# Kernel tuning notes

Hardware: AMD Instinct MI355X
Metric: run time of the kernel (lower is better)

Reference implementation:

```python
import jax, jax.numpy as jnp
import numpy as np

B, S, N = 8, 32, 64
F_NODE = 32
TRI = N * (N - 1) // 2        # 2016 upper-triangular edge features per step
DIN = F_NODE + TRI            # 2048 GATConv input dim (node feats + broadcast edge feats)
H, DOUT = 4, 256              # num_heads, hidden_channels
R = 1024                      # rnn_hidden_size
OUT = TRI                     # edge_in_channels * N*(N-1)/2


def setup_inputs() -> dict:
    key = jax.random.key(0)
    ks = jax.random.split(key, 16)
    def nrm(k, shape, fan):
        return jax.random.normal(k, shape, jnp.float32) / np.float32(np.sqrt(fan))
    # complete directed graph (no self loops; GATConv adds them)
    idx = np.arange(N)
    src = np.repeat(idx, N); dst = np.tile(idx, N)
    keep = src != dst
    edge_index = jnp.asarray(np.stack([src[keep], dst[keep]]), dtype=jnp.int32)  # [2, 4032]
    return {
        "x_node": jax.random.normal(ks[0], (B, S, N, F_NODE), jnp.float32),
        "x_edge": jax.random.normal(ks[1], (B, S, TRI), jnp.float32),
        "edge_index": edge_index,
        "W_gat": nrm(ks[2], (DIN, H * DOUT), DIN),
        "att_src": nrm(ks[3], (H, DOUT), DOUT),
        "att_dst": nrm(ks[4], (H, DOUT), DOUT),
        "b_gat": jnp.zeros((DOUT,), jnp.float32),
        "W_ih0": nrm(ks[5], (3 * R, N * DOUT), N * DOUT),
        "W_hh0": nrm(ks[6], (3 * R, R), R),
        "b_ih0": jnp.zeros((3 * R,), jnp.float32),
        "b_hh0": jnp.zeros((3 * R,), jnp.float32),
        "W_ih1": nrm(ks[7], (3 * R, R), R),
        "W_hh1": nrm(ks[8], (3 * R, R), R),
        "b_ih1": jnp.zeros((3 * R,), jnp.float32),
        "b_hh1": jnp.zeros((3 * R,), jnp.float32),
        "W_fc": nrm(ks[9], (R, OUT), R),
        "b_fc": jnp.zeros((OUT,), jnp.float32),
    }


def _gru_layer(x, Wih, Whh, bih, bhh):
    # x: [B, S, D] -> [B, S, R], PyTorch GRU equations
    def step(h, xt):
        gi = xt @ Wih.T + bih
        gh = h @ Whh.T + bhh
        i_r, i_z, i_n = jnp.split(gi, 3, axis=-1)
        h_r, h_z, h_n = jnp.split(gh, 3, axis=-1)
        r = jax.nn.sigmoid(i_r + h_r)
        z = jax.nn.sigmoid(i_z + h_z)
        n = jnp.tanh(i_n + r * h_n)
        h = (1.0 - z) * n + z * h
        return h, h
    h0 = jnp.zeros((x.shape[0], Whh.shape[1]), x.dtype)
    _, ys = jax.lax.scan(step, h0, jnp.swapaxes(x, 0, 1))
    return jnp.swapaxes(ys, 0, 1)


def reference(x_node, x_edge, edge_index, W_gat, att_src, att_dst, b_gat,
              W_ih0, W_hh0, b_ih0, b_hh0, W_ih1, W_hh1, b_ih1, b_hh1, W_fc, b_fc):
    # concat node feats with per-step edge features broadcast to every node
    x = jnp.concatenate(
        [x_node, jnp.broadcast_to(x_edge[:, :, None, :], (B, S, N, TRI))], axis=-1)
    xg = x.reshape(B * S, N, DIN)                         # batch all (b,t) graphs
    h = (xg @ W_gat).reshape(B * S, N, H, DOUT)           # per-head projections
    a_s = jnp.einsum('bnhe,he->bnh', h, att_src)
    a_d = jnp.einsum('bnhe,he->bnh', h, att_dst)
    # edge (src j -> dst i): leaky_relu(a_src[j] + a_dst[i]); dense over [dst, src]
    scores = jax.nn.leaky_relu(a_d[:, :, None, :] + a_s[:, None, :, :], 0.2)  # [BS, i, j, H]
    adj = jnp.zeros((N, N), bool).at[edge_index[1], edge_index[0]].set(True)
    adj = adj.at[jnp.arange(N), jnp.arange(N)].set(True)  # GATConv add_self_loops=True
    scores = jnp.where(adj[None, :, :, None], scores, -jnp.inf)
    alpha = jax.nn.softmax(scores, axis=2)                # softmax over source neighbors
    gat = jnp.einsum('bish,bshe->bihe', alpha, h).mean(axis=2) + b_gat  # concat=False -> head mean
    gat = jax.nn.relu(gat)                                # [BS, N, DOUT]
    seq = gat.reshape(B, S, N * DOUT)
    y = _gru_layer(seq, W_ih0, W_hh0, b_ih0, b_hh0)
    y = _gru_layer(y, W_ih1, W_hh1, b_ih1, b_hh1)
    return y[:, -1] @ W_fc + b_fc                         # [B, OUT]
```

## Files before the change

### kernel.cpp

```cpp
#include <hip/hip_runtime.h>
#include <hip/hip_bf16.h>

using bf16 = __hip_bfloat16;
typedef __bf16 bf16x8 __attribute__((ext_vector_type(8)));
typedef float f32x4 __attribute__((ext_vector_type(4)));


__device__ __forceinline__ void unp2(unsigned int u, float& a, float& b) {
  a = __uint_as_float(u << 16);
  b = __uint_as_float(u & 0xffff0000u);
}

__device__ __forceinline__ bf16x8 cvt8(float4 a, float4 b) {
  bf16x8 r;
  r[0] = (__bf16)a.x; r[1] = (__bf16)a.y; r[2] = (__bf16)a.z; r[3] = (__bf16)a.w;
  r[4] = (__bf16)b.x; r[5] = (__bf16)b.y; r[6] = (__bf16)b.z; r[7] = (__bf16)b.w;
  return r;
}

__global__ __launch_bounds__(256) void gru_step2_k(
    const float* __restrict__ X,
    const float* __restrict__ Whh,
    const float* __restrict__ bhh,
    float* __restrict__ y,
    int s, int first) {
  __shared__ float hs[8][1024];
  const int tid = threadIdx.x;
  if (first) {
#pragma unroll
    for (int q = 0; q < 8; ++q) {
      int idx = q * 256 + tid;
      *(float4*)&hs[idx >> 8][(idx & 255) * 4] = make_float4(0.f, 0.f, 0.f, 0.f);
    }
  } else {
#pragma unroll
    for (int q = 0; q < 8; ++q) {
      int idx = q * 256 + tid;
      int b = idx >> 8, kf = (idx & 255) * 4;
      *(float4*)&hs[b][kf] =
          *(const float4*)&y[(size_t)(b * 32 + s - 1) * 1024 + kf];
    }
  }
  __syncthreads();
  const int wv = tid >> 6, lane = tid & 63;
  const int j = blockIdx.x * 4 + wv;
  const float* Wr = Whh + (size_t)j * 1024;
  const float* Wz = Whh + (size_t)(1024 + j) * 1024;
  const float* Wn = Whh + (size_t)(2048 + j) * 1024;
  float accR[8] = {}, accZ[8] = {}, accN[8] = {};
#pragma unroll
  for (int kk = 0; kk < 4; ++kk) {
    const int k = kk * 256 + lane * 4;
    float4 wr = *(const float4*)&Wr[k];
    float4 wz = *(const float4*)&Wz[k];
    float4 wn = *(const float4*)&Wn[k];
#pragma unroll
    for (int b = 0; b < 8; ++b) {
      float4 h4 = *(const float4*)&hs[b][k];
      accR[b] += h4.x * wr.x + h4.y * wr.y + h4.z * wr.z + h4.w * wr.w;
      accZ[b] += h4.x * wz.x + h4.y * wz.y + h4.z * wz.z + h4.w * wz.w;
      accN[b] += h4.x * wn.x + h4.y * wn.y + h4.z * wn.z + h4.w * wn.w;
    }
  }
#pragma unroll
  for (int d = 1; d < 64; d <<= 1) {
#pragma unroll
    for (int b = 0; b < 8; ++b) {
      accR[b] += __shfl_xor(accR[b], d);
      accZ[b] += __shfl_xor(accZ[b], d);
      accN[b] += __shfl_xor(accN[b], d);
    }
  }
  if (lane < 8) {
    const int b = lane;
    float sr = 0.f, sz = 0.f, sn = 0.f;
#pragma unroll
    for (int bb = 0; bb < 8; ++bb)
      if (b == bb) { sr = accR[bb]; sz = accZ[bb]; sn = accN[bb]; }
    const float* gip = X + (size_t)(b * 32 + s) * 3072;
    float r = 1.0f / (1.0f + __expf(-(gip[j] + sr + bhh[j])));
    float z = 1.0f / (1.0f + __expf(-(gip[1024 + j] + sz + bhh[1024 + j])));
    float n = tanhf(gip[2048 + j] + r * (sn + bhh[2048 + j]));
    float hp = hs[b][j];
    y[(size_t)(b * 32 + s) * 1024 + j] = (1.0f - z) * n + z * hp;
  }
}

__global__ __launch_bounds__(256) void gemm_bt16_k(const __bf16* __restrict__ A,
                                                   const float* __restrict__ Bm,
                                                   float* __restrict__ Cp,
                                                   int N, int K, int ksper) {
  __shared__ __bf16 As[256][40];
  __shared__ __bf16 Bs[128][40];
  const int tid = threadIdx.x;
  const int bn = blockIdx.x * 128;
  const int lane = tid & 63, wv = tid >> 6;
  const int wr = wv >> 1, wc = wv & 1;
  const int lr = lane & 15, kh = lane >> 4;
  const int brow = tid >> 1, bhalf = tid & 1;
  f32x4 acc[8][4] = {};
  const int kstot = K >> 5;
  int ks0 = blockIdx.z * ksper;
  int ks1 = ks0 + ksper; if (ks1 > kstot) ks1 = kstot;
  uint4 ra0, ra1, ra2, ra3; float4 rb0, rb1, rb2, rb3;
  {
    const int k0 = ks0 << 5;
    const uint4* ap = (const uint4*)(A + (size_t)tid * K + k0);
    ra0 = ap[0]; ra1 = ap[1]; ra2 = ap[2]; ra3 = ap[3];
    const float* bp = Bm + (size_t)(bn + brow) * K + k0 + bhalf * 16;
    rb0 = ((const float4*)bp)[0]; rb1 = ((const float4*)bp)[1];
    rb2 = ((const float4*)bp)[2]; rb3 = ((const float4*)bp)[3];
  }
  for (int ks = ks0; ks < ks1; ++ks) {
    __syncthreads();
    *(uint4*)&As[tid][0]  = ra0;
    *(uint4*)&As[tid][8]  = ra1;
    *(uint4*)&As[tid][16] = ra2;
    *(uint4*)&As[tid][24] = ra3;
    *(bf16x8*)&Bs[brow][bhalf * 16] = cvt8(rb0, rb1);
    *(bf16x8*)&Bs[brow][bhalf * 16 + 8] = cvt8(rb2, rb3);
    __syncthreads();
    if (ks + 1 < ks1) {
      const int k0 = (ks + 1) << 5;
      const uint4* ap = (const uint4*)(A + (size_t)tid * K + k0);
      ra0 = ap[0]; ra1 = ap[1]; ra2 = ap[2]; ra3 = ap[3];
      const float* bp = Bm + (size_t)(bn + brow) * K + k0 + bhalf * 16;
      rb0 = ((const float4*)bp)[0]; rb1 = ((const float4*)bp)[1];
      rb2 = ((const float4*)bp)[2]; rb3 = ((const float4*)bp)[3];
    }
    bf16x8 bfv[4];
#pragma unroll
    for (int ni = 0; ni < 4; ++ni)
      bfv[ni] = *(const bf16x8*)&Bs[wc * 64 + ni * 16 + lr][kh * 8];
#pragma unroll
    for (int mi = 0; mi < 8; ++mi) {
      bf16x8 af = *(const bf16x8*)&As[wr * 128 + mi * 16 + lr][kh * 8];
#pragma unroll
      for (int ni = 0; ni < 4; ++ni)
        acc[mi][ni] = __builtin_amdgcn_mfma_f32_16x16x32_bf16(af, bfv[ni],
                                                              acc[mi][ni], 0, 0, 0);
    }
  }
  float* cp = Cp + (size_t)blockIdx.z * 256 * N;
#pragma unroll
  for (int mi = 0; mi < 8; ++mi) {
#pragma unroll
    for (int ni = 0; ni < 4; ++ni) {
      const int row = wr * 128 + mi * 16 + kh * 4;
      const int col = bn + wc * 64 + ni * 16 + lr;
#pragma unroll
      for (int j = 0; j < 4; ++j)
        cp[(size_t)(row + j) * N + col] = acc[mi][ni][j];
    }
  }
}

template <bool BT>
__global__ __launch_bounds__(256) void mfma_gemm_k(const float* __restrict__ A,
                                                   const float* __restrict__ Bm,
                                                   float* __restrict__ Cp,
                                                   int M, int N, int K,
                                                   int lda, int ldb, int ksper) {
  __shared__ __bf16 As[128][40];
  __shared__ __bf16 Bs[128][40];
  const int tid = threadIdx.x;
  const int bm = blockIdx.y * 128, bn = blockIdx.x * 128;
  const int lane = tid & 63, wv = tid >> 6;
  const int wr = wv >> 1, wc = wv & 1;
  const int lr = lane & 15, kh = lane >> 4;
  f32x4 acc[4][4] = {};
  const int kstot = K >> 5;
  int ks0 = blockIdx.z * ksper;
  int ks1 = ks0 + ksper; if (ks1 > kstot) ks1 = kstot;
  for (int ks = ks0; ks < ks1; ++ks) {
    const int k0 = ks << 5;
    __syncthreads();
    {
      const int row = tid >> 1, half = tid & 1;
      const float* ap = A + (size_t)(bm + row) * lda + k0 + half * 16;
      float4 f0 = ((const float4*)ap)[0], f1 = ((const float4*)ap)[1];
      float4 f2 = ((const float4*)ap)[2], f3 = ((const float4*)ap)[3];
      *(bf16x8*)&As[row][half * 16] = cvt8(f0, f1);
      *(bf16x8*)&As[row][half * 16 + 8] = cvt8(f2, f3);
    }
    if (BT) {
      const int row = tid >> 1, half = tid & 1;
      const float* bp = Bm + (size_t)(bn + row) * ldb + k0 + half * 16;
      float4 f0 = ((const float4*)bp)[0], f1 = ((const float4*)bp)[1];
      float4 f2 = ((const float4*)bp)[2], f3 = ((const float4*)bp)[3];
      *(bf16x8*)&Bs[row][half * 16] = cvt8(f0, f1);
      *(bf16x8*)&Bs[row][half * 16 + 8] = cvt8(f2, f3);
    } else {
      const int kk = tid >> 3, ng = tid & 7;
      const float* bp = Bm + (size_t)(k0 + kk) * ldb + bn + ng * 16;
      float4 f[4];
#pragma unroll
      for (int q = 0; q < 4; ++q) f[q] = ((const float4*)bp)[q];
#pragma unroll
      for (int q = 0; q < 4; ++q) {
        Bs[ng * 16 + q * 4 + 0][kk] = (__bf16)f[q].x;
        Bs[ng * 16 + q * 4 + 1][kk] = (__bf16)f[q].y;
        Bs[ng * 16 + q * 4 + 2][kk] = (__bf16)f[q].z;
        Bs[ng * 16 + q * 4 + 3][kk] = (__bf16)f[q].w;
      }
    }
    __syncthreads();
    bf16x8 af[4], bfv[4];
#pragma unroll
    for (int mi = 0; mi < 4; ++mi)
      af[mi] = *(const bf16x8*)&As[wr * 64 + mi * 16 + lr][kh * 8];
#pragma unroll
    for (int ni = 0; ni < 4; ++ni)
      bfv[ni] = *(const bf16x8*)&Bs[wc * 64 + ni * 16 + lr][kh * 8];
#pragma unroll
    for (int mi = 0; mi < 4; ++mi)
#pragma unroll
      for (int ni = 0; ni < 4; ++ni)
        acc[mi][ni] = __builtin_amdgcn_mfma_f32_16x16x32_bf16(af[mi], bfv[ni],
                                                              acc[mi][ni], 0, 0, 0);
  }
  float* cp = Cp + (size_t)blockIdx.z * M * N;
#pragma unroll
  for (int mi = 0; mi < 4; ++mi) {
#pragma unroll
    for (int ni = 0; ni < 4; ++ni) {
      const int row = bm + wr * 64 + mi * 16 + kh * 4;
      const int col = bn + wc * 64 + ni * 16 + lr;
#pragma unroll
      for (int j = 0; j < 4; ++j)
        cp[(size_t)(row + j) * N + col] = acc[mi][ni][j];
    }
  }
}

__global__ __launch_bounds__(256) void reduce_k(const float* __restrict__ Cp,
                                                const float* __restrict__ bias,
                                                float* __restrict__ C,
                                                int MN, int N, int nsk) {
  int i = (blockIdx.x * 256 + threadIdx.x) * 4;
  if (i >= MN) return;
  float4 s = make_float4(0.f, 0.f, 0.f, 0.f);
  if (bias) s = *(const float4*)&bias[i % N];
  for (int sk = 0; sk < nsk; ++sk) {
    float4 p = *(const float4*)&Cp[(size_t)sk * MN + i];
    s.x += p.x; s.y += p.y; s.z += p.z; s.w += p.w;
  }
  *(float4*)&C[i] = s;
}

__global__ __launch_bounds__(256) void node_h_k(const float* __restrict__ xn,
                                                const float* __restrict__ Wg,
                                                const float* __restrict__ he,
                                                bf16* __restrict__ hbuf) {
  __shared__ float xns[64][32];
  __shared__ float wgs[32][256];
  const int cq = blockIdx.x, g = blockIdx.y;
  const int tid = threadIdx.x;
  for (int idx = tid; idx < 2048; idx += 256) xns[idx >> 5][idx & 31] = xn[g * 2048 + idx];
  for (int r = 0; r < 32; ++r) wgs[r][tid] = Wg[r * 1024 + cq * 256 + tid];
  __syncthreads();
  const float hev = he[g * 1024 + cq * 256 + tid];
  for (int n0 = 0; n0 < 64; n0 += 8) {
    float acc[8];
#pragma unroll
    for (int nn = 0; nn < 8; ++nn) acc[nn] = hev;
    for (int f = 0; f < 32; ++f) {
      float w = wgs[f][tid];
#pragma unroll
      for (int nn = 0; nn < 8; ++nn) acc[nn] += xns[n0 + nn][f] * w;
    }
#pragma unroll
    for (int nn = 0; nn < 8; ++nn)
      hbuf[(size_t)(g * 64 + n0 + nn) * 1024 + cq * 256 + tid] = __float2bfloat16(acc[nn]);
  }
}

__global__ __launch_bounds__(256) void as_ad_k(const bf16* __restrict__ hbuf,
                                               const float* __restrict__ att_s,
                                               const float* __restrict__ att_d,
                                               float* __restrict__ as_o,
                                               float* __restrict__ ad_o) {
  const int tid = threadIdx.x;
  const int lane = tid & 63, wv = tid >> 6;
  const int row = blockIdx.x * 4 + wv;
  const int hd = lane >> 4;
  const int e0 = (lane & 15) * 16;
  float as_r[16], ad_r[16];
#pragma unroll
  for (int q = 0; q < 4; ++q) {
    float4 v = *(const float4*)(att_s + hd * 256 + e0 + q * 4);
    as_r[q * 4 + 0] = v.x; as_r[q * 4 + 1] = v.y; as_r[q * 4 + 2] = v.z; as_r[q * 4 + 3] = v.w;
    float4 w = *(const float4*)(att_d + hd * 256 + e0 + q * 4);
    ad_r[q * 4 + 0] = w.x; ad_r[q * 4 + 1] = w.y; ad_r[q * 4 + 2] = w.z; ad_r[q * 4 + 3] = w.w;
  }
  const uint4* hp = (const uint4*)(hbuf + (size_t)row * 1024 + lane * 16);
  uint4 p0 = hp[0], p1 = hp[1];
  float hv[16];
  unp2(p0.x, hv[0], hv[1]);  unp2(p0.y, hv[2], hv[3]);
  unp2(p0.z, hv[4], hv[5]);  unp2(p0.w, hv[6], hv[7]);
  unp2(p1.x, hv[8], hv[9]);  unp2(p1.y, hv[10], hv[11]);
  unp2(p1.z, hv[12], hv[13]); unp2(p1.w, hv[14], hv[15]);
  float ps = 0.f, pd = 0.f;
#pragma unroll
  for (int i = 0; i < 16; ++i) { ps += as_r[i] * hv[i]; pd += ad_r[i] * hv[i]; }
#pragma unroll
  for (int m = 1; m < 16; m <<= 1) { ps += __shfl_xor(ps, m); pd += __shfl_xor(pd, m); }
  if ((lane & 15) == 0) { as_o[row * 4 + hd] = ps; ad_o[row * 4 + hd] = pd; }
}

__global__ __launch_bounds__(256) void attn_agg_k(const bf16* __restrict__ hbuf,
                                                  const float* __restrict__ as_i,
                                                  const float* __restrict__ ad_i,
                                                  const float* __restrict__ bgat,
                                                  __bf16* __restrict__ seq) {
  __shared__ float ass[256], ads[256], bgs[256];
  __shared__ float alpha[4][64][64];
  __shared__ float hq[64][260];
  const int g = blockIdx.x, tid = threadIdx.x;
  ass[tid] = as_i[g * 256 + tid];
  ads[tid] = ad_i[g * 256 + tid];
  bgs[tid] = bgat[tid];
  __syncthreads();
  {
    const int hd = tid >> 6, i = tid & 63;
    const float ad = ads[i * 4 + hd];
    float m = -1e30f;
    for (int j = 0; j < 64; ++j) {
      float s = ad + ass[j * 4 + hd];
      s = s > 0.0f ? s : 0.2f * s;
      m = fmaxf(m, s);
    }
    float sum = 0.0f;
    for (int j = 0; j < 64; ++j) {
      float s = ad + ass[j * 4 + hd];
      s = s > 0.0f ? s : 0.2f * s;
      sum += __expf(s - m);
    }
    const float inv = 1.0f / sum;
    for (int j = 0; j < 64; ++j) {
      float s = ad + ass[j * 4 + hd];
      s = s > 0.0f ? s : 0.2f * s;
      alpha[hd][j][i] = __expf(s - m) * inv;
    }
  }
  const int i = tid & 63, eq = tid >> 6;
  float acc[64] = {};
  for (int hd = 0; hd < 4; ++hd) {
    __syncthreads();
    for (int idx = tid; idx < 2048; idx += 256) {
      int j = idx >> 5, ch = idx & 31;
      uint4 p = *(const uint4*)(hbuf + (size_t)(g * 64 + j) * 1024 + hd * 256 + ch * 8);
      float f0, f1, f2, f3, f4, f5, f6, f7;
      unp2(p.x, f0, f1); unp2(p.y, f2, f3); unp2(p.z, f4, f5); unp2(p.w, f6, f7);
      *(float4*)&hq[j][ch * 8] = make_float4(f0, f1, f2, f3);
      *(float4*)&hq[j][ch * 8 + 4] = make_float4(f4, f5, f6, f7);
    }
    __syncthreads();
    for (int j = 0; j < 64; ++j) {
      const float a = alpha[hd][j][i];
      const float* hr = &hq[j][eq * 64];
#pragma unroll
      for (int q = 0; q < 16; ++q) {
        float4 hv = *(const float4*)(hr + q * 4);
        acc[q * 4 + 0] += a * hv.x; acc[q * 4 + 1] += a * hv.y;
        acc[q * 4 + 2] += a * hv.z; acc[q * 4 + 3] += a * hv.w;
      }
    }
  }
  __bf16* op = seq + (size_t)g * 16384 + i * 256 + eq * 64;
#pragma unroll
  for (int q = 0; q < 8; ++q) {
    float4 lo, hi;
    lo.x = fmaxf(bgs[eq * 64 + q * 8 + 0] + 0.25f * acc[q * 8 + 0], 0.0f);
    lo.y = fmaxf(bgs[eq * 64 + q * 8 + 1] + 0.25f * acc[q * 8 + 1], 0.0f);
    lo.z = fmaxf(bgs[eq * 64 + q * 8 + 2] + 0.25f * acc[q * 8 + 2], 0.0f);
    lo.w = fmaxf(bgs[eq * 64 + q * 8 + 3] + 0.25f * acc[q * 8 + 3], 0.0f);
    hi.x = fmaxf(bgs[eq * 64 + q * 8 + 4] + 0.25f * acc[q * 8 + 4], 0.0f);
    hi.y = fmaxf(bgs[eq * 64 + q * 8 + 5] + 0.25f * acc[q * 8 + 5], 0.0f);
    hi.z = fmaxf(bgs[eq * 64 + q * 8 + 6] + 0.25f * acc[q * 8 + 6], 0.0f);
    hi.w = fmaxf(bgs[eq * 64 + q * 8 + 7] + 0.25f * acc[q * 8 + 7], 0.0f);
    *(bf16x8*)(op + q * 8) = cvt8(lo, hi);
  }
}

__global__ __launch_bounds__(256) void fc_k(const float* __restrict__ y1,
                                            const float* __restrict__ Wfc,
                                            const float* __restrict__ bfc,
                                            float* __restrict__ out) {
  __shared__ float As[8][1024];
  const int tid = threadIdx.x;
  for (int idx = tid; idx < 8192; idx += 256) {
    int b = idx >> 10, k = idx & 1023;
    As[b][k] = y1[(size_t)(b * 32 + 31) * 1024 + k];
  }
  __syncthreads();
  const int ol = tid >> 2, kq = tid & 3;
  const int o = blockIdx.x * 64 + ol;
  float acc[8] = {};
  if (o < 2016) {
    for (int i2 = 0; i2 < 256; ++i2) {
      int k = i2 * 4 + kq;
      float w = Wfc[(size_t)k * 2016 + o];
#pragma unroll
      for (int b = 0; b < 8; ++b) acc[b] += As[b][k] * w;
    }
  }
#pragma unroll
  for (int b = 0; b < 8; ++b) {
    acc[b] += __shfl_xor(acc[b], 1);
    acc[b] += __shfl_xor(acc[b], 2);
  }
  if (kq == 0 && o < 2016) {
#pragma unroll
    for (int b = 0; b < 8; ++b) out[b * 2016 + o] = acc[b] + bfc[o];
  }
}

extern "C" void kernel_launch(void* const* d_in, const int* in_sizes, int n_in,
                              void* d_out, int out_size, void* d_ws, size_t ws_size,
                              hipStream_t stream) {
  (void)in_sizes; (void)n_in; (void)out_size; (void)ws_size;
  const float* x_node = (const float*)d_in[0];
  const float* x_edge = (const float*)d_in[1];
  const float* W_gat = (const float*)d_in[3];
  const float* att_s = (const float*)d_in[4];
  const float* att_d = (const float*)d_in[5];
  const float* b_gat = (const float*)d_in[6];
  const float* W_ih0 = (const float*)d_in[7];
  const float* W_hh0 = (const float*)d_in[8];
  const float* b_ih0 = (const float*)d_in[9];
  const float* b_hh0 = (const float*)d_in[10];
  const float* W_ih1 = (const float*)d_in[11];
  const float* W_hh1 = (const float*)d_in[12];
  const float* b_ih1 = (const float*)d_in[13];
  const float* b_hh1 = (const float*)d_in[14];
  const float* W_fc  = (const float*)d_in[15];
  const float* b_fc  = (const float*)d_in[16];

  char* ws = (char*)d_ws;
  size_t off = 0;
  float*  he  = (float*)(ws + off);  off += 256u * 1024 * 4;
  float*  a_s = (float*)(ws + off);  off += 256u * 64 * 4 * 4;
  float*  a_d = (float*)(ws + off);  off += 256u * 64 * 4 * 4;
  bf16*   hb  = (bf16*)(ws + off);   off += 256u * 64 * 1024 * 2;
  __bf16* seq = (__bf16*)(ws + off); off += 256u * 16384 * 2;
  float*  X0  = (float*)(ws + off);  off += 256u * 3072 * 4;
  float*  y0  = (float*)(ws + off);  off += 256u * 1024 * 4;
  float*  X1  = (float*)(ws + off);  off += 256u * 3072 * 4;
  float*  y1  = (float*)(ws + off);  off += 256u * 1024 * 4;
  off = (off + 255) & ~(size_t)255;
  float*  Cp  = (float*)(ws + off);  off += (size_t)16 * 256 * 3072 * 4;

  mfma_gemm_k<false><<<dim3(8, 2, 8), 256, 0, stream>>>(
      x_edge, W_gat + 32 * 1024, Cp, 256, 1024, 2016, 2016, 1024, 8);
  reduce_k<<<256, 256, 0, stream>>>(Cp, nullptr, he, 256 * 1024, 1024, 8);
  node_h_k<<<dim3(4, 256), 256, 0, stream>>>(x_node, W_gat, he, hb);
  as_ad_k<<<4096, 256, 0, stream>>>(hb, att_s, att_d, a_s, a_d);
  attn_agg_k<<<256, 256, 0, stream>>>(hb, a_s, a_d, b_gat, seq);
  gemm_bt16_k<<<dim3(24, 1, 16), 256, 0, stream>>>(seq, W_ih0, Cp,
                                                   3072, 16384, 32);
  reduce_k<<<768, 256, 0, stream>>>(Cp, b_ih0, X0, 256 * 3072, 3072, 16);
  for (int s = 0; s < 32; ++s)
    gru_step2_k<<<256, 256, 0, stream>>>(X0, W_hh0, b_hh0, y0, s, s == 0 ? 1 : 0);
  mfma_gemm_k<true><<<dim3(24, 2, 4), 256, 0, stream>>>(
      y0, W_ih1, Cp, 256, 3072, 1024, 1024, 1024, 8);
  reduce_k<<<768, 256, 0, stream>>>(Cp, b_ih1, X1, 256 * 3072, 3072, 4);
  for (int s = 0; s < 32; ++s)
    gru_step2_k<<<256, 256, 0, stream>>>(X1, W_hh1, b_hh1, y1, s, s == 0 ? 1 : 0);
  fc_k<<<32, 256, 0, stream>>>(y1, W_fc, b_fc, (float*)d_out);
}
```

Baseline: 665.6 us.

## Replace per-step GRU launches with persistent kernel using grid barrier

The 32 per-timestep GRU kernel launches per layer become one persistent kernel that loops over timesteps. Blocks synchronise through a flag-based grid barrier in global memory, with block 0 acting as the releaser, which removes per-launch overhead and relaunch gaps. The bf16 GEMM k-loop is also restructured into a two-stage ping-pong register prefetch. The barrier relies on all 256 blocks being co-resident, which holds on this GPU but would deadlock otherwise. Its relaxed atomics carry no explicit fences, so the ordering of the y writes is not guaranteed by the memory model.

Result: slower. 852.2 us (+28.0%).

```diff
diff --git a/kernel.cpp b/kernel.cpp
--- a/kernel.cpp
+++ b/kernel.cpp
@@ -18,71 +18,106 @@
   return r;
 }
 
-__global__ __launch_bounds__(256) void gru_step2_k(
+__device__ __forceinline__ float ald(const float* p) {
+  return __hip_atomic_load(p, __ATOMIC_RELAXED, __HIP_MEMORY_SCOPE_AGENT);
+}
+__device__ __forceinline__ void ast(float* p, float v) {
+  __hip_atomic_store(p, v, __ATOMIC_RELAXED, __HIP_MEMORY_SCOPE_AGENT);
+}
+__device__ __forceinline__ unsigned uald(const unsigned* p) {
+  return __hip_atomic_load(p, __ATOMIC_RELAXED, __HIP_MEMORY_SCOPE_AGENT);
+}
+__device__ __forceinline__ void uast(unsigned* p, unsigned v) {
+  __hip_atomic_store(p, v, __ATOMIC_RELAXED, __HIP_MEMORY_SCOPE_AGENT);
+}
+
+__global__ __launch_bounds__(256) void gru_persist2_k(
     const float* __restrict__ X,
     const float* __restrict__ Whh,
     const float* __restrict__ bhh,
     float* __restrict__ y,
-    int s, int first) {
+    unsigned* __restrict__ flags,
+    unsigned* __restrict__ rel) {
   __shared__ float hs[8][1024];
   const int tid = threadIdx.x;
-  if (first) {
-#pragma unroll
-    for (int q = 0; q < 8; ++q) {
-      int idx = q * 256 + tid;
-      *(float4*)&hs[idx >> 8][(idx & 255) * 4] = make_float4(0.f, 0.f, 0.f, 0.f);
-    }
-  } else {
-#pragma unroll
-    for (int q = 0; q < 8; ++q) {
-      int idx = q * 256 + tid;
-      int b = idx >> 8, kf = (idx & 255) * 4;
-      *(float4*)&hs[b][kf] =
-          *(const float4*)&y[(size_t)(b * 32 + s - 1) * 1024 + kf];
-    }
-  }
-  __syncthreads();
+  const int bid = blockIdx.x;
   const int wv = tid >> 6, lane = tid & 63;
-  const int j = blockIdx.x * 4 + wv;
+  const int j = bid * 4 + wv;
   const float* Wr = Whh + (size_t)j * 1024;
   const float* Wz = Whh + (size_t)(1024 + j) * 1024;
   const float* Wn = Whh + (size_t)(2048 + j) * 1024;
-  float accR[8] = {}, accZ[8] = {}, accN[8] = {};
-#pragma unroll
-  for (int kk = 0; kk < 4; ++kk) {
-    const int k = kk * 256 + lane * 4;
-    float4 wr = *(const float4*)&Wr[k];
-    float4 wz = *(const float4*)&Wz[k];
-    float4 wn = *(const float4*)&Wn[k];
-#pragma unroll
-    for (int b = 0; b < 8; ++b) {
-      float4 h4 = *(const float4*)&hs[b][k];
-      accR[b] += h4.x * wr.x + h4.y * wr.y + h4.z * wr.z + h4.w * wr.w;
-      accZ[b] += h4.x * wz.x + h4.y * wz.y + h4.z * wz.z + h4.w * wz.w;
-      accN[b] += h4.x * wn.x + h4.y * wn.y + h4.z * wn.z + h4.w * wn.w;
-    }
-  }
-#pragma unroll
-  for (int d = 1; d < 64; d <<= 1) {
-#pragma unroll
-    for (int b = 0; b < 8; ++b) {
-      accR[b] += __shfl_xor(accR[b], d);
-      accZ[b] += __shfl_xor(accZ[b], d);
-      accN[b] += __shfl_xor(accN[b], d);
-    }
-  }
-  if (lane < 8) {
-    const int b = lane;
-    float sr = 0.f, sz = 0.f, sn = 0.f;
-#pragma unroll
-    for (int bb = 0; bb < 8; ++bb)
-      if (b == bb) { sr = accR[bb]; sz = accZ[bb]; sn = accN[bb]; }
-    const float* gip = X + (size_t)(b * 32 + s) * 3072;
-    float r = 1.0f / (1.0f + __expf(-(gip[j] + sr + bhh[j])));
-    float z = 1.0f / (1.0f + __expf(-(gip[1024 + j] + sz + bhh[1024 + j])));
-    float n = tanhf(gip[2048 + j] + r * (sn + bhh[2048 + j]));
-    float hp = hs[b][j];
-    y[(size_t)(b * 32 + s) * 1024 + j] = (1.0f - z) * n + z * hp;
+  const float bhr = bhh[j], bhz = bhh[1024 + j], bhn = bhh[2048 + j];
+  for (int s = 0; s < 32; ++s) {
+    if (s == 0) {
+#pragma unroll
+      for (int q = 0; q < 8; ++q) {
+        int idx = q * 256 + tid;
+        *(float4*)&hs[idx >> 8][(idx & 255) * 4] = make_float4(0.f, 0.f, 0.f, 0.f);
+      }
+    } else {
+#pragma unroll
+      for (int q = 0; q < 8; ++q) {
+        int idx = q * 256 + tid;
+        int b = idx >> 8, kf = (idx & 255) * 4;
+        const float* hp_ = y + (size_t)(b * 32 + s - 1) * 1024 + kf;
+        float4 v;
+        v.x = ald(hp_ + 0); v.y = ald(hp_ + 1);
+        v.z = ald(hp_ + 2); v.w = ald(hp_ + 3);
+        *(float4*)&hs[b][kf] = v;
+      }
+    }
+    __syncthreads();
+    float accR[8] = {}, accZ[8] = {}, accN[8] = {};
+#pragma unroll
+    for (int kk = 0; kk < 4; ++kk) {
+      const int k = kk * 256 + lane * 4;
+      float4 wr = *(const float4*)&Wr[k];
+      float4 wz = *(const float4*)&Wz[k];
+      float4 wn = *(const float4*)&Wn[k];
+#pragma unroll
+      for (int b = 0; b < 8; ++b) {
+        float4 h4 = *(const float4*)&hs[b][k];
+        accR[b] += h4.x * wr.x + h4.y * wr.y + h4.z * wr.z + h4.w * wr.w;
+        accZ[b] += h4.x * wz.x + h4.y * wz.y + h4.z * wz.z + h4.w * wz.w;
+        accN[b] += h4.x * wn.x + h4.y * wn.y + h4.z * wn.z + h4.w * wn.w;
+      }
+    }
+#pragma unroll
+    for (int d = 1; d < 64; d <<= 1) {
+#pragma unroll
+      for (int b = 0; b < 8; ++b) {
+        accR[b] += __shfl_xor(accR[b], d);
+        accZ[b] += __shfl_xor(accZ[b], d);
+        accN[b] += __shfl_xor(accN[b], d);
+      }
+    }
+    if (lane < 8) {
+      const int b = lane;
+      float sr = 0.f, sz = 0.f, sn = 0.f;
+#pragma unroll
+      for (int bb = 0; bb < 8; ++bb)
+        if (b == bb) { sr = accR[bb]; sz = accZ[bb]; sn = accN[bb]; }
+      const float* gip = X + (size_t)(b * 32 + s) * 3072;
+      float r = 1.0f / (1.0f + __expf(-(gip[j] + sr + bhr)));
+      float z = 1.0f / (1.0f + __expf(-(gip[1024 + j] + sz + bhz)));
+      float n = tanhf(gip[2048 + j] + r * (sn + bhn));
+      float hp = hs[b][j];
+      ast(&y[(size_t)(b * 32 + s) * 1024 + j], (1.0f - z) * n + z * hp);
+    }
+    if (s < 31) {
+      const unsigned ep = (unsigned)(s + 1);
+      __syncthreads();
+      if (tid == 0) uast(&flags[bid * 16], ep);
+      if (bid == 0) {
+        while (uald(&flags[tid * 16]) != ep) __builtin_amdgcn_s_sleep(1);
+        __syncthreads();
+        if (tid == 0) uast(&rel[s * 16], 1u);
+      }
+      if (tid == 0) {
+        while (uald(&rel[s * 16]) == 0u) __builtin_amdgcn_s_sleep(1);
+      }
+      __syncthreads();
+    }
   }
 }
 
@@ -99,35 +134,41 @@
   const int lr = lane & 15, kh = lane >> 4;
   const int brow = tid >> 1, bhalf = tid & 1;
   f32x4 acc[8][4] = {};
-  const int kstot = K >> 5;
-  int ks0 = blockIdx.z * ksper;
-  int ks1 = ks0 + ksper; if (ks1 > kstot) ks1 = kstot;
-  uint4 ra0, ra1, ra2, ra3; float4 rb0, rb1, rb2, rb3;
-  {
-    const int k0 = ks0 << 5;
+  const int ks0 = blockIdx.z * ksper;
+  const int ks1 = ks0 + ksper;
+
+  uint4 xa0, xa1, xa2, xa3; float4 xb0, xb1, xb2, xb3;
+  uint4 ya0, ya1, ya2, ya3; float4 yb0, yb1, yb2, yb3;
+
+  auto loadX = [&](int ks) {
+    const int k0 = ks << 5;
     const uint4* ap = (const uint4*)(A + (size_t)tid * K + k0);
-    ra0 = ap[0]; ra1 = ap[1]; ra2 = ap[2]; ra3 = ap[3];
+    xa0 = ap[0]; xa1 = ap[1]; xa2 = ap[2]; xa3 = ap[3];
     const float* bp = Bm + (size_t)(bn + brow) * K + k0 + bhalf * 16;
-    rb0 = ((const float4*)bp)[0]; rb1 = ((const float4*)bp)[1];
-    rb2 = ((const float4*)bp)[2]; rb3 = ((const float4*)bp)[3];
-  }
-  for (int ks = ks0; ks < ks1; ++ks) {
-    __syncthreads();
-    *(uint4*)&As[tid][0]  = ra0;
-    *(uint4*)&As[tid][8]  = ra1;
-    *(uint4*)&As[tid][16] = ra2;
-    *(uint4*)&As[tid][24] = ra3;
-    *(bf16x8*)&Bs[brow][bhalf * 16] = cvt8(rb0, rb1);
-    *(bf16x8*)&Bs[brow][bhalf * 16 + 8] = cvt8(rb2, rb3);
-    __syncthreads();
-    if (ks + 1 < ks1) {
-      const int k0 = (ks + 1) << 5;
-      const uint4* ap = (const uint4*)(A + (size_t)tid * K + k0);
-      ra0 = ap[0]; ra1 = ap[1]; ra2 = ap[2]; ra3 = ap[3];
-      const float* bp = Bm + (size_t)(bn + brow) * K + k0 + bhalf * 16;
-      rb0 = ((const float4*)bp)[0]; rb1 = ((const float4*)bp)[1];
-      rb2 = ((const float4*)bp)[2]; rb3 = ((const float4*)bp)[3];
-    }
+    xb0 = ((const float4*)bp)[0]; xb1 = ((const float4*)bp)[1];
+    xb2 = ((const float4*)bp)[2]; xb3 = ((const float4*)bp)[3];
+  };
+  auto loadY = [&](int ks) {
+    const int k0 = ks << 5;
+    const uint4* ap = (const uint4*)(A + (size_t)tid * K + k0);
+    ya0 = ap[0]; ya1 = ap[1]; ya2 = ap[2]; ya3 = ap[3];
+    const float* bp = Bm + (size_t)(bn + brow) * K + k0 + bhalf * 16;
+    yb0 = ((const float4*)bp)[0]; yb1 = ((const float4*)bp)[1];
+    yb2 = ((const float4*)bp)[2]; yb3 = ((const float4*)bp)[3];
+  };
+  auto storeX = [&]() {
+    *(uint4*)&As[tid][0]  = xa0; *(uint4*)&As[tid][8]  = xa1;
+    *(uint4*)&As[tid][16] = xa2; *(uint4*)&As[tid][24] = xa3;
+    *(bf16x8*)&Bs[brow][bhalf * 16] = cvt8(xb0, xb1);
+    *(bf16x8*)&Bs[brow][bhalf * 16 + 8] = cvt8(xb2, xb3);
+  };
+  auto storeY = [&]() {
+    *(uint4*)&As[tid][0]  = ya0; *(uint4*)&As[tid][8]  = ya1;
+    *(uint4*)&As[tid][16] = ya2; *(uint4*)&As[tid][24] = ya3;
+    *(bf16x8*)&Bs[brow][bhalf * 16] = cvt8(yb0, yb1);
+    *(bf16x8*)&Bs[brow][bhalf * 16 + 8] = cvt8(yb2, yb3);
+  };
+  auto mfmaLDS = [&]() {
     bf16x8 bfv[4];
 #pragma unroll
     for (int ni = 0; ni < 4; ++ni)
@@ -140,6 +181,21 @@
         acc[mi][ni] = __builtin_amdgcn_mfma_f32_16x16x32_bf16(af, bfv[ni],
                                                               acc[mi][ni], 0, 0, 0);
     }
+  };
+
+  loadX(ks0);
+  loadY(ks0 + 1);
+  for (int ks = ks0; ks < ks1; ks += 2) {
+    __syncthreads();
+    storeX();
+    __syncthreads();
+    { int nk = ks + 2; if (nk >= ks1) nk = ks1 - 1; loadX(nk); }
+    mfmaLDS();
+    __syncthreads();
+    storeY();
+    __syncthreads();
+    { int nk = ks + 3; if (nk >= ks1) nk = ks1 - 1; loadY(nk); }
+    mfmaLDS();
   }
   float* cp = Cp + (size_t)blockIdx.z * 256 * N;
 #pragma unroll
@@ -149,8 +205,8 @@
       const int row = wr * 128 + mi * 16 + kh * 4;
       const int col = bn + wc * 64 + ni * 16 + lr;
 #pragma unroll
-      for (int j = 0; j < 4; ++j)
-        cp[(size_t)(row + j) * N + col] = acc[mi][ni][j];
+      for (int jj = 0; jj < 4; ++jj)
+        cp[(size_t)(row + jj) * N + col] = acc[mi][ni][jj];
     }
   }
 }
@@ -449,6 +505,8 @@
   float*  X1  = (float*)(ws + off);  off += 256u * 3072 * 4;
   float*  y1  = (float*)(ws + off);  off += 256u * 1024 * 4;
   off = (off + 255) & ~(size_t)255;
+  unsigned* flags = (unsigned*)(ws + off); off += 256u * 64;
+  unsigned* rel   = (unsigned*)(ws + off); off += 32u * 64;
   float*  Cp  = (float*)(ws + off);  off += (size_t)16 * 256 * 3072 * 4;
 
   mfma_gemm_k<false><<<dim3(8, 2, 8), 256, 0, stream>>>(
@@ -460,12 +518,12 @@
   gemm_bt16_k<<<dim3(24, 1, 16), 256, 0, stream>>>(seq, W_ih0, Cp,
                                                    3072, 16384, 32);
   reduce_k<<<768, 256, 0, stream>>>(Cp, b_ih0, X0, 256 * 3072, 3072, 16);
-  for (int s = 0; s < 32; ++s)
-    gru_step2_k<<<256, 256, 0, stream>>>(X0, W_hh0, b_hh0, y0, s, s == 0 ? 1 : 0);
+  hipMemsetAsync(flags, 0, 256u * 64 + 32u * 64, stream);
+  gru_persist2_k<<<256, 256, 0, stream>>>(X0, W_hh0, b_hh0, y0, flags, rel);
   mfma_gemm_k<true><<<dim3(24, 2, 4), 256, 0, stream>>>(
       y0, W_ih1, Cp, 256, 3072, 1024, 1024, 1024, 8);
   reduce_k<<<768, 256, 0, stream>>>(Cp, b_ih1, X1, 256 * 3072, 3072, 4);
-  for (int s = 0; s < 32; ++s)
-    gru_step2_k<<<256, 256, 0, stream>>>(X1, W_hh1, b_hh1, y1, s, s == 0 ? 1 : 0);
+  hipMemsetAsync(flags, 0, 256u * 64 + 32u * 64, stream);
+  gru_persist2_k<<<256, 256, 0, stream>>>(X1, W_hh1, b_hh1, y1, flags, rel);
   fc_k<<<32, 256, 0, stream>>>(y1, W_fc, b_fc, (float*)d_out);
 }
```

## Wavefront-pipeline both GRU layers in one fused per-step kernel

Applied to the files above, without the earlier changes.

Fuses the two GRU layers into a single kernel launched 33 times. Layer 0 step t runs alongside layer 1 step t-1, and layer 1 computes its input projection inline instead of through a separate GEMM and reduce. This roughly halves the number of sequential step launches and drops the layer-1 input GEMM, reduce and X1 buffer. In exchange, layer 1 now does its input projection in fp32 FMA per step and reads W_ih1 and W_hh1 every step, with 512 blocks each using 64KB of LDS.

Measured after the change: 765.4 us. +15.0%, slower.

```diff
diff --git a/kernel.cpp b/kernel.cpp
--- a/kernel.cpp
+++ b/kernel.cpp
@@ -18,71 +18,150 @@
   return r;
 }
 
-__global__ __launch_bounds__(256) void gru_step2_k(
-    const float* __restrict__ X,
-    const float* __restrict__ Whh,
-    const float* __restrict__ bhh,
-    float* __restrict__ y,
-    int s, int first) {
-  __shared__ float hs[8][1024];
+__global__ __launch_bounds__(256) void gru_fused_k(
+    const float* __restrict__ X0,
+    const float* __restrict__ Whh0,
+    const float* __restrict__ bhh0,
+    float* __restrict__ y0,
+    const float* __restrict__ Wih1,
+    const float* __restrict__ bih1,
+    const float* __restrict__ Whh1,
+    const float* __restrict__ bhh1,
+    float* __restrict__ y1,
+    int t) {
+  __shared__ float sA[8][1024];
+  __shared__ float sB[8][1024];
   const int tid = threadIdx.x;
-  if (first) {
-#pragma unroll
-    for (int q = 0; q < 8; ++q) {
-      int idx = q * 256 + tid;
-      *(float4*)&hs[idx >> 8][(idx & 255) * 4] = make_float4(0.f, 0.f, 0.f, 0.f);
+  const int wv = tid >> 6, lane = tid & 63;
+
+  if (blockIdx.x < 256) {
+    if (t >= 32) return;
+    const int s = t;
+    if (s == 0) {
+#pragma unroll
+      for (int q = 0; q < 8; ++q) {
+        int idx = q * 256 + tid;
+        *(float4*)&sA[idx >> 8][(idx & 255) * 4] = make_float4(0.f, 0.f, 0.f, 0.f);
+      }
+    } else {
+#pragma unroll
+      for (int q = 0; q < 8; ++q) {
+        int idx = q * 256 + tid;
+        int b = idx >> 8, kf = (idx & 255) * 4;
+        *(float4*)&sA[b][kf] =
+            *(const float4*)&y0[(size_t)(b * 32 + s - 1) * 1024 + kf];
+      }
+    }
+    __syncthreads();
+    const int j = blockIdx.x * 4 + wv;
+    const float* Wr = Whh0 + (size_t)j * 1024;
+    const float* Wz = Whh0 + (size_t)(1024 + j) * 1024;
+    const float* Wn = Whh0 + (size_t)(2048 + j) * 1024;
+    float accR[8] = {}, accZ[8] = {}, accN[8] = {};
+#pragma unroll
+    for (int kk = 0; kk < 4; ++kk) {
+      const int k = kk * 256 + lane * 4;
+      float4 wr = *(const float4*)&Wr[k];
+      float4 wz = *(const float4*)&Wz[k];
+      float4 wn = *(const float4*)&Wn[k];
+#pragma unroll
+      for (int b = 0; b < 8; ++b) {
+        float4 h4 = *(const float4*)&sA[b][k];
+        accR[b] += h4.x * wr.x + h4.y * wr.y + h4.z * wr.z + h4.w * wr.w;
+        accZ[b] += h4.x * wz.x + h4.y * wz.y + h4.z * wz.z + h4.w * wz.w;
+        accN[b] += h4.x * wn.x + h4.y * wn.y + h4.z * wn.z + h4.w * wn.w;
+      }
+    }
+#pragma unroll
+    for (int d = 1; d < 64; d <<= 1) {
+#pragma unroll
+      for (int b = 0; b < 8; ++b) {
+        accR[b] += __shfl_xor(accR[b], d);
+        accZ[b] += __shfl_xor(accZ[b], d);
+        accN[b] += __shfl_xor(accN[b], d);
+      }
+    }
+    if (lane < 8) {
+      const int b = lane;
+      float sr = 0.f, sz = 0.f, sn = 0.f;
+#pragma unroll
+      for (int bb = 0; bb < 8; ++bb)
+        if (b == bb) { sr = accR[bb]; sz = accZ[bb]; sn = accN[bb]; }
+      const float* gip = X0 + (size_t)(b * 32 + s) * 3072;
+      float r = 1.0f / (1.0f + __expf(-(gip[j] + sr + bhh0[j])));
+      float z = 1.0f / (1.0f + __expf(-(gip[1024 + j] + sz + bhh0[1024 + j])));
+      float n = tanhf(gip[2048 + j] + r * (sn + bhh0[2048 + j]));
+      float hp = sA[b][j];
+      y0[(size_t)(b * 32 + s) * 1024 + j] = (1.0f - z) * n + z * hp;
     }
   } else {
-#pragma unroll
-    for (int q = 0; q < 8; ++q) {
-      int idx = q * 256 + tid;
-      int b = idx >> 8, kf = (idx & 255) * 4;
-      *(float4*)&hs[b][kf] =
-          *(const float4*)&y[(size_t)(b * 32 + s - 1) * 1024 + kf];
-    }
-  }
-  __syncthreads();
-  const int wv = tid >> 6, lane = tid & 63;
-  const int j = blockIdx.x * 4 + wv;
-  const float* Wr = Whh + (size_t)j * 1024;
-  const float* Wz = Whh + (size_t)(1024 + j) * 1024;
-  const float* Wn = Whh + (size_t)(2048 + j) * 1024;
-  float accR[8] = {}, accZ[8] = {}, accN[8] = {};
-#pragma unroll
-  for (int kk = 0; kk < 4; ++kk) {
-    const int k = kk * 256 + lane * 4;
-    float4 wr = *(const float4*)&Wr[k];
-    float4 wz = *(const float4*)&Wz[k];
-    float4 wn = *(const float4*)&Wn[k];
-#pragma unroll
-    for (int b = 0; b < 8; ++b) {
-      float4 h4 = *(const float4*)&hs[b][k];
-      accR[b] += h4.x * wr.x + h4.y * wr.y + h4.z * wr.z + h4.w * wr.w;
-      accZ[b] += h4.x * wz.x + h4.y * wz.y + h4.z * wz.z + h4.w * wz.w;
-      accN[b] += h4.x * wn.x + h4.y * wn.y + h4.z * wn.z + h4.w * wn.w;
-    }
-  }
-#pragma unroll
-  for (int d = 1; d < 64; d <<= 1) {
-#pragma unroll
-    for (int b = 0; b < 8; ++b) {
-      accR[b] += __shfl_xor(accR[b], d);
-      accZ[b] += __shfl_xor(accZ[b], d);
-      accN[b] += __shfl_xor(accN[b], d);
-    }
-  }
-  if (lane < 8) {
-    const int b = lane;
-    float sr = 0.f, sz = 0.f, sn = 0.f;
-#pragma unroll
-    for (int bb = 0; bb < 8; ++bb)
-      if (b == bb) { sr = accR[bb]; sz = accZ[bb]; sn = accN[bb]; }
-    const float* gip = X + (size_t)(b * 32 + s) * 3072;
-    float r = 1.0f / (1.0f + __expf(-(gip[j] + sr + bhh[j])));
-    float z = 1.0f / (1.0f + __expf(-(gip[1024 + j] + sz + bhh[1024 + j])));
-    float n = tanhf(gip[2048 + j] + r * (sn + bhh[2048 + j]));
-    float hp = hs[b][j];
-    y[(size_t)(b * 32 + s) * 1024 + j] = (1.0f - z) * n + z * hp;
+    if (t < 1) return;
+    const int s = t - 1;
+    {
+#pragma unroll
+      for (int q = 0; q < 8; ++q) {
+        int idx = q * 256 + tid;
+        int b = idx >> 8, kf = (idx & 255) * 4;
+        *(float4*)&sA[b][kf] =
+            *(const float4*)&y0[(size_t)(b * 32 + s) * 1024 + kf];
+        float4 v = make_float4(0.f, 0.f, 0.f, 0.f);
+        if (s > 0)
+          v = *(const float4*)&y1[(size_t)(b * 32 + s - 1) * 1024 + kf];
+        *(float4*)&sB[b][kf] = v;
+      }
+    }
+    __syncthreads();
+    const int j = (blockIdx.x - 256) * 4 + wv;
+    const float* WiR = Wih1 + (size_t)j * 1024;
+    const float* WiZ = Wih1 + (size_t)(1024 + j) * 1024;
+    const float* WiN = Wih1 + (size_t)(2048 + j) * 1024;
+    const float* WhR = Whh1 + (size_t)j * 1024;
+    const float* WhZ = Whh1 + (size_t)(1024 + j) * 1024;
+    const float* WhN = Whh1 + (size_t)(2048 + j) * 1024;
+    float accRZ[8] = {}, accZZ[8] = {}, accIN[8] = {}, accHN[8] = {};
+#pragma unroll
+    for (int kk = 0; kk < 4; ++kk) {
+      const int k = kk * 256 + lane * 4;
+      float4 wir = *(const float4*)&WiR[k];
+      float4 wiz = *(const float4*)&WiZ[k];
+      float4 win = *(const float4*)&WiN[k];
+      float4 whr = *(const float4*)&WhR[k];
+      float4 whz = *(const float4*)&WhZ[k];
+      float4 whn = *(const float4*)&WhN[k];
+#pragma unroll
+      for (int b = 0; b < 8; ++b) {
+        float4 x4 = *(const float4*)&sA[b][k];
+        float4 h4 = *(const float4*)&sB[b][k];
+        accRZ[b] += x4.x * wir.x + x4.y * wir.y + x4.z * wir.z + x4.w * wir.w
+                  + h4.x * whr.x + h4.y * whr.y + h4.z * whr.z + h4.w * whr.w;
+        accZZ[b] += x4.x * wiz.x + x4.y * wiz.y + x4.z * wiz.z + x4.w * wiz.w
+                  + h4.x * whz.x + h4.y * whz.y + h4.z * whz.z + h4.w * whz.w;
+        accIN[b] += x4.x * win.x + x4.y * win.y + x4.z * win.z + x4.w * win.w;
+        accHN[b] += h4.x * whn.x + h4.y * whn.y + h4.z * whn.z + h4.w * whn.w;
+      }
+    }
+#pragma unroll
+    for (int d = 1; d < 64; d <<= 1) {
+#pragma unroll
+      for (int b = 0; b < 8; ++b) {
+        accRZ[b] += __shfl_xor(accRZ[b], d);
+        accZZ[b] += __shfl_xor(accZZ[b], d);
+        accIN[b] += __shfl_xor(accIN[b], d);
+        accHN[b] += __shfl_xor(accHN[b], d);
+      }
+    }
+    if (lane < 8) {
+      const int b = lane;
+      float srz = 0.f, szz = 0.f, sin_ = 0.f, shn = 0.f;
+#pragma unroll
+      for (int bb = 0; bb < 8; ++bb)
+        if (b == bb) { srz = accRZ[bb]; szz = accZZ[bb]; sin_ = accIN[bb]; shn = accHN[bb]; }
+      float r = 1.0f / (1.0f + __expf(-(srz + bih1[j] + bhh1[j])));
+      float z = 1.0f / (1.0f + __expf(-(szz + bih1[1024 + j] + bhh1[1024 + j])));
+      float n = tanhf(sin_ + bih1[2048 + j] + r * (shn + bhh1[2048 + j]));
+      float hp = sB[b][j];
+      y1[(size_t)(b * 32 + s) * 1024 + j] = (1.0f - z) * n + z * hp;
+    }
   }
 }
 
@@ -446,7 +525,6 @@
   __bf16* seq = (__bf16*)(ws + off); off += 256u * 16384 * 2;
   float*  X0  = (float*)(ws + off);  off += 256u * 3072 * 4;
   float*  y0  = (float*)(ws + off);  off += 256u * 1024 * 4;
-  float*  X1  = (float*)(ws + off);  off += 256u * 3072 * 4;
   float*  y1  = (float*)(ws + off);  off += 256u * 1024 * 4;
   off = (off + 255) & ~(size_t)255;
   float*  Cp  = (float*)(ws + off);  off += (size_t)16 * 256 * 3072 * 4;
@@ -460,12 +538,8 @@
   gemm_bt16_k<<<dim3(24, 1, 16), 256, 0, stream>>>(seq, W_ih0, Cp,
                                                    3072, 16384, 32);
   reduce_k<<<768, 256, 0, stream>>>(Cp, b_ih0, X0, 256 * 3072, 3072, 16);
-  for (int s = 0; s < 32; ++s)
-    gru_step2_k<<<256, 256, 0, stream>>>(X0, W_hh0, b_hh0, y0, s, s == 0 ? 1 : 0);
-  mfma_gemm_k<true><<<dim3(24, 2, 4), 256, 0, stream>>>(
-      y0, W_ih1, Cp, 256, 3072, 1024, 1024, 1024, 8);
-  reduce_k<<<768, 256, 0, stream>>>(Cp, b_ih1, X1, 256 * 3072, 3072, 4);
-  for (int s = 0; s < 32; ++s)
-    gru_step2_k<<<256, 256, 0, stream>>>(X1, W_hh1, b_hh1, y1, s, s == 0 ? 1 : 0);
+  for (int t = 0; t <= 32; ++t)
+    gru_fused_k<<<512, 256, 0, stream>>>(X0, W_hh0, b_hh0, y0,
+                                         W_ih1, b_ih1, W_hh1, b_hh1, y1, t);
   fc_k<<<32, 256, 0, stream>>>(y1, W_fc, b_fc, (float*)d_out);
 }
```

## Split GRU step across batch halves and double split-K for input GEMM

Applied to the files above, without the earlier changes.

The recurrent GRU step kernel now splits the batch into two halves per block, launching 512 blocks instead of 256. Each wave assigns 16-lane groups to individual batch rows, which cuts per-thread accumulators from 24 to 3 and shortens the shuffle reduction. The cost is that each W_hh row is read twice, once per batch half. Separately, the layer-0 input GEMM uses 32 K-splits instead of 16, with a larger partial buffer and reduction, to put more blocks in flight.

Result: slower. 698.0 us (+4.9%).

```diff
diff --git a/kernel.cpp b/kernel.cpp
--- a/kernel.cpp
+++ b/kernel.cpp
@@ -18,70 +18,63 @@
   return r;
 }
 
-__global__ __launch_bounds__(256) void gru_step2_k(
+__global__ __launch_bounds__(256) void gru_step3_k(
     const float* __restrict__ X,
     const float* __restrict__ Whh,
     const float* __restrict__ bhh,
     float* __restrict__ y,
     int s, int first) {
-  __shared__ float hs[8][1024];
-  const int tid = threadIdx.x;
+  __shared__ float hs[4][1028];
+  const int tid = threadIdx.x;
+  const int bh = blockIdx.x & 1;
+  const int jg = blockIdx.x >> 1;
   if (first) {
 #pragma unroll
-    for (int q = 0; q < 8; ++q) {
+    for (int q = 0; q < 4; ++q) {
       int idx = q * 256 + tid;
       *(float4*)&hs[idx >> 8][(idx & 255) * 4] = make_float4(0.f, 0.f, 0.f, 0.f);
     }
   } else {
 #pragma unroll
-    for (int q = 0; q < 8; ++q) {
+    for (int q = 0; q < 4; ++q) {
       int idx = q * 256 + tid;
-      int b = idx >> 8, kf = (idx & 255) * 4;
-      *(float4*)&hs[b][kf] =
-          *(const float4*)&y[(size_t)(b * 32 + s - 1) * 1024 + kf];
+      int bl = idx >> 8, kf = (idx & 255) * 4;
+      *(float4*)&hs[bl][kf] =
+          *(const float4*)&y[(size_t)((bh * 4 + bl) * 32 + s - 1) * 1024 + kf];
     }
   }
   __syncthreads();
   const int wv = tid >> 6, lane = tid & 63;
-  const int j = blockIdx.x * 4 + wv;
+  const int j = jg * 4 + wv;
+  const int bl = lane >> 4, kg = lane & 15;
   const float* Wr = Whh + (size_t)j * 1024;
   const float* Wz = Whh + (size_t)(1024 + j) * 1024;
   const float* Wn = Whh + (size_t)(2048 + j) * 1024;
-  float accR[8] = {}, accZ[8] = {}, accN[8] = {};
-#pragma unroll
-  for (int kk = 0; kk < 4; ++kk) {
-    const int k = kk * 256 + lane * 4;
+  float aR = 0.f, aZ = 0.f, aN = 0.f;
+#pragma unroll
+  for (int q = 0; q < 16; ++q) {
+    const int k = q * 64 + kg * 4;
     float4 wr = *(const float4*)&Wr[k];
     float4 wz = *(const float4*)&Wz[k];
     float4 wn = *(const float4*)&Wn[k];
-#pragma unroll
-    for (int b = 0; b < 8; ++b) {
-      float4 h4 = *(const float4*)&hs[b][k];
-      accR[b] += h4.x * wr.x + h4.y * wr.y + h4.z * wr.z + h4.w * wr.w;
-      accZ[b] += h4.x * wz.x + h4.y * wz.y + h4.z * wz.z + h4.w * wz.w;
-      accN[b] += h4.x * wn.x + h4.y * wn.y + h4.z * wn.z + h4.w * wn.w;
-    }
-  }
-#pragma unroll
-  for (int d = 1; d < 64; d <<= 1) {
-#pragma unroll
-    for (int b = 0; b < 8; ++b) {
-      accR[b] += __shfl_xor(accR[b], d);
-      accZ[b] += __shfl_xor(accZ[b], d);
-      accN[b] += __shfl_xor(accN[b], d);
-    }
-  }
-  if (lane < 8) {
-    const int b = lane;
-    float sr = 0.f, sz = 0.f, sn = 0.f;
-#pragma unroll
-    for (int bb = 0; bb < 8; ++bb)
-      if (b == bb) { sr = accR[bb]; sz = accZ[bb]; sn = accN[bb]; }
+    float4 h4 = *(const float4*)&hs[bl][k];
+    aR += h4.x * wr.x + h4.y * wr.y + h4.z * wr.z + h4.w * wr.w;
+    aZ += h4.x * wz.x + h4.y * wz.y + h4.z * wz.z + h4.w * wz.w;
+    aN += h4.x * wn.x + h4.y * wn.y + h4.z * wn.z + h4.w * wn.w;
+  }
+#pragma unroll
+  for (int d = 1; d < 16; d <<= 1) {
+    aR += __shfl_xor(aR, d);
+    aZ += __shfl_xor(aZ, d);
+    aN += __shfl_xor(aN, d);
+  }
+  if (kg == 0) {
+    const int b = bh * 4 + bl;
     const float* gip = X + (size_t)(b * 32 + s) * 3072;
-    float r = 1.0f / (1.0f + __expf(-(gip[j] + sr + bhh[j])));
-    float z = 1.0f / (1.0f + __expf(-(gip[1024 + j] + sz + bhh[1024 + j])));
-    float n = tanhf(gip[2048 + j] + r * (sn + bhh[2048 + j]));
-    float hp = hs[b][j];
+    float r = 1.0f / (1.0f + __expf(-(gip[j] + aR + bhh[j])));
+    float z = 1.0f / (1.0f + __expf(-(gip[1024 + j] + aZ + bhh[1024 + j])));
+    float n = tanhf(gip[2048 + j] + r * (aN + bhh[2048 + j]));
+    float hp = hs[bl][j];
     y[(size_t)(b * 32 + s) * 1024 + j] = (1.0f - z) * n + z * hp;
   }
 }
@@ -449,7 +442,7 @@
   float*  X1  = (float*)(ws + off);  off += 256u * 3072 * 4;
   float*  y1  = (float*)(ws + off);  off += 256u * 1024 * 4;
   off = (off + 255) & ~(size_t)255;
-  float*  Cp  = (float*)(ws + off);  off += (size_t)16 * 256 * 3072 * 4;
+  float*  Cp  = (float*)(ws + off);  off += (size_t)32 * 256 * 3072 * 4;
 
   mfma_gemm_k<false><<<dim3(8, 2, 8), 256, 0, stream>>>(
       x_edge, W_gat + 32 * 1024, Cp, 256, 1024, 2016, 2016, 1024, 8);
@@ -457,15 +450,15 @@
   node_h_k<<<dim3(4, 256), 256, 0, stream>>>(x_node, W_gat, he, hb);
   as_ad_k<<<4096, 256, 0, stream>>>(hb, att_s, att_d, a_s, a_d);
   attn_agg_k<<<256, 256, 0, stream>>>(hb, a_s, a_d, b_gat, seq);
-  gemm_bt16_k<<<dim3(24, 1, 16), 256, 0, stream>>>(seq, W_ih0, Cp,
-                                                   3072, 16384, 32);
-  reduce_k<<<768, 256, 0, stream>>>(Cp, b_ih0, X0, 256 * 3072, 3072, 16);
+  gemm_bt16_k<<<dim3(24, 1, 32), 256, 0, stream>>>(seq, W_ih0, Cp,
+                                                   3072, 16384, 16);
+  reduce_k<<<768, 256, 0, stream>>>(Cp, b_ih0, X0, 256 * 3072, 3072, 32);
   for (int s = 0; s < 32; ++s)
-    gru_step2_k<<<256, 256, 0, stream>>>(X0, W_hh0, b_hh0, y0, s, s == 0 ? 1 : 0);
+    gru_step3_k<<<512, 256, 0, stream>>>(X0, W_hh0, b_hh0, y0, s, s == 0 ? 1 : 0);
   mfma_gemm_k<true><<<dim3(24, 2, 4), 256, 0, stream>>>(
       y0, W_ih1, Cp, 256, 3072, 1024, 1024, 1024, 8);
   reduce_k<<<768, 256, 0, stream>>>(Cp, b_ih1, X1, 256 * 3072, 3072, 4);
   for (int s = 0; s < 32; ++s)
-    gru_step2_k<<<256, 256, 0, stream>>>(X1, W_hh1, b_hh1, y1, s, s == 0 ? 1 : 0);
+    gru_step3_k<<<512, 256, 0, stream>>>(X1, W_hh1, b_hh1, y1, s, s == 0 ? 1 : 0);
   fc_k<<<32, 256, 0, stream>>>(y1, W_fc, b_fc, (float*)d_out);
 }
```
